# Optimization experiments

Measured on AMD Instinct MI355X. Metric: run time of the kernel, lower is better.

Reference implementation:

```python
import jax, jax.numpy as jnp
import numpy as np
from jax import lax

IMAGE_SIZE = 1280
STRIDE = 32
FMP = IMAGE_SIZE // STRIDE          # 40
BPC = 5                             # boxes per cell (5 anchors)
NUM_CLASSES = 80
NMS_THRESH = 0.5
CONF_THRESH = 0.3
N_BOX = FMP * FMP * BPC             # 8000 candidates
ANCHOR_SIZE = np.array([[17, 25], [55, 75], [92, 206], [202, 21], [289, 311]], dtype=np.float32)


def _make_anchors():
    # generate_anchors: per-cell (x,y) grid repeated for each of BPC anchors, tiled anchor wh
    ys, xs = jnp.meshgrid(jnp.arange(FMP, dtype=jnp.float32), jnp.arange(FMP, dtype=jnp.float32), indexing='ij')
    xy = jnp.stack([xs, ys], axis=-1).reshape(-1, 1, 2)                       # [HW,1,2]
    anchor_xy = jnp.broadcast_to(xy, (FMP * FMP, BPC, 2)).reshape(-1, 2)      # [N,2]
    anchor_wh = jnp.broadcast_to(jnp.asarray(ANCHOR_SIZE)[None], (FMP * FMP, BPC, 2)).reshape(-1, 2)
    return jnp.concatenate([anchor_xy, anchor_wh], axis=-1)                   # [N,4]


def setup_inputs() -> dict:
    key = jax.random.key(0)
    k = jax.random.split(key, 5)
    return {
        'cls_feat': jax.random.normal(k[0], (1, 512, FMP, FMP), jnp.float32),
        'reg_feat': jax.random.normal(k[1], (1, 512, FMP, FMP), jnp.float32),
        'w_obj': jax.random.normal(k[2], (BPC, 512), jnp.float32) * 0.02,
        'b_obj': jnp.zeros((BPC,), jnp.float32),
        'w_cls': jax.random.normal(k[3], (NUM_CLASSES * BPC, 512), jnp.float32) * 0.02,
        'b_cls': jnp.zeros((NUM_CLASSES * BPC,), jnp.float32),
        'w_reg': jax.random.normal(k[4], (4 * BPC, 512), jnp.float32) * 0.02,
        'b_reg': jnp.zeros((4 * BPC,), jnp.float32),
    }


def reference(cls_feat, reg_feat, w_obj, b_obj, w_cls, b_cls, w_reg, b_reg):
    # 1x1 convs as channel contractions, already permuted to NHWC like permute(0,2,3,1)
    obj = (jnp.einsum('bchw,oc->bhwo', reg_feat, w_obj) + b_obj).reshape(-1, 1)            # [N,1]
    cls = (jnp.einsum('bchw,oc->bhwo', cls_feat, w_cls) + b_cls).reshape(-1, NUM_CLASSES)  # [N,C]
    reg = (jnp.einsum('bchw,oc->bhwo', reg_feat, w_reg) + b_reg).reshape(-1, 4)            # [N,4]

    scores = jnp.sqrt(jax.nn.sigmoid(obj) * jax.nn.sigmoid(cls))                           # [N,C]

    # decode_boxes
    anchors = _make_anchors()
    ctr = (jax.nn.sigmoid(reg[:, :2]) + anchors[:, :2]) * STRIDE
    wh = jnp.exp(reg[:, 2:]) * anchors[:, 2:]
    bboxes = jnp.concatenate([ctr - wh * 0.5, ctr + wh * 0.5], axis=-1)                    # [N,4] x1y1x2y2

    # postprocess: per-box best class + confidence filter
    labels = jnp.argmax(scores, axis=1)
    score = jnp.take_along_axis(scores, labels[:, None], axis=1)[:, 0]
    valid = score >= CONF_THRESH

    # faithful to original nms(): it re-interprets decoded x1y1x2y2 as cxcywh before IoU
    b2 = jnp.concatenate([bboxes[:, :2] - bboxes[:, 2:] * 0.5,
                          bboxes[:, :2] + bboxes[:, 2:] * 0.5], axis=-1)

    # greedy per-class NMS == global greedy with cross-class IoU gated to 0
    order = jnp.argsort(-score)
    bs = b2[order]
    ls = labels[order]
    vs = valid[order]
    areas = (bs[:, 2] - bs[:, 0]) * (bs[:, 3] - bs[:, 1])
    xx1 = jnp.maximum(bs[:, None, 0], bs[None, :, 0])
    yy1 = jnp.maximum(bs[:, None, 1], bs[None, :, 1])
    xx2 = jnp.minimum(bs[:, None, 2], bs[None, :, 2])
    yy2 = jnp.minimum(bs[:, None, 3], bs[None, :, 3])
    inter = jnp.maximum(1e-10, xx2 - xx1) * jnp.maximum(1e-10, yy2 - yy1)
    iou = inter / (areas[:, None] + areas[None, :] - inter + 1e-14)                        # [N,N]
    same = ls[:, None] == ls[None, :]

    idx = jnp.arange(N_BOX)

    def body(k, supp):
        active = vs[k] & jnp.logical_not(supp[k])
        row = active & (iou[k] > NMS_THRESH) & same[k] & (idx > k)
        return supp | row

    supp = lax.fori_loop(0, N_BOX, body, jnp.zeros(N_BOX, bool))
    keep = jnp.zeros(N_BOX, bool).at[order].set(vs & jnp.logical_not(supp))

    # fixed-size masked outputs (original returns variable-length filtered arrays)
    return bboxes, score, labels, keep
```

## Files before the change

### kernel.cpp

```cpp
#include <hip/hip_runtime.h>
#include <math.h>

#define FMPX 40
#define NPOS 1600
#define NCLS 80
#define NBOX 8000
#define KDIM 512
#define CAP  256

__constant__ float c_aw[5] = {17.f, 55.f, 92.f, 202.f, 289.f};
__constant__ float c_ah[5] = {25.f, 75.f, 206.f, 21.f, 311.f};

__device__ __forceinline__ float sigf(float x) { return 1.0f / (1.0f + expf(-x)); }

__global__ __launch_bounds__(256) void k_gemm(
    const float* __restrict__ cls_feat, const float* __restrict__ reg_feat,
    const float* __restrict__ w_obj, const float* __restrict__ b_obj,
    const float* __restrict__ w_cls, const float* __restrict__ b_cls,
    const float* __restrict__ w_reg, const float* __restrict__ b_reg,
    float* __restrict__ clsRaw,
    float* __restrict__ roRaw)
{
    __shared__ float Ws[16 * KDIM];
    const int mTile = blockIdx.x;
    const int nTile = blockIdx.y;
    const int hw0   = mTile * 64;
    const bool isCls = (nTile < 25);
    const float* feat = isCls ? cls_feat : reg_feat;

    const int pos = threadIdx.x & 63;
    const int og  = threadIdx.x >> 6;

    const float* ap = feat + hw0 + pos;

    float A0[8], A1[8];
#pragma unroll
    for (int t = 0; t < 8; t++) A0[t] = ap[t * NPOS];
#pragma unroll
    for (int t = 0; t < 8; t++) A1[t] = ap[(8 + t) * NPOS];

    for (int i = threadIdx.x * 4; i < 16 * KDIM; i += 256 * 4) {
        int r = i >> 9, k = i & 511;
        const float* src;
        bool valid = true;
        if (isCls) {
            src = w_cls + (nTile * 16 + r) * KDIM + k;
        } else {
            int o = (nTile - 25) * 16 + r;
            if (o < 5)       src = w_obj + o * KDIM + k;
            else if (o < 25) src = w_reg + (o - 5) * KDIM + k;
            else           { src = w_obj; valid = false; }
        }
        float4 v = valid ? *(const float4*)src : make_float4(0.f, 0.f, 0.f, 0.f);
        *(float4*)&Ws[i] = v;
    }

    float bias[4];
    bool ok[4];
#pragma unroll
    for (int j = 0; j < 4; j++) {
        int r = og * 4 + j;
        if (isCls) {
            bias[j] = b_cls[nTile * 16 + r]; ok[j] = true;
        } else {
            int o = (nTile - 25) * 16 + r;
            if (o < 5)       { bias[j] = b_obj[o];     ok[j] = true; }
            else if (o < 25) { bias[j] = b_reg[o - 5]; ok[j] = true; }
            else             { bias[j] = 0.0f;         ok[j] = false; }
        }
    }

    __syncthreads();

    float acc[4] = {0.f, 0.f, 0.f, 0.f};
    const float* wsBase = &Ws[(og * 4) * KDIM];

    for (int kk = 0; kk < KDIM - 16; kk += 16) {
#pragma unroll
        for (int j = 0; j < 4; j++) {
            const float* wp = wsBase + j * KDIM + kk;
            acc[j] += A0[0] * wp[0]; acc[j] += A0[1] * wp[1];
            acc[j] += A0[2] * wp[2]; acc[j] += A0[3] * wp[3];
            acc[j] += A0[4] * wp[4]; acc[j] += A0[5] * wp[5];
            acc[j] += A0[6] * wp[6]; acc[j] += A0[7] * wp[7];
        }
#pragma unroll
        for (int t = 0; t < 8; t++) A0[t] = ap[(kk + 16 + t) * NPOS];
#pragma unroll
        for (int j = 0; j < 4; j++) {
            const float* wp = wsBase + j * KDIM + kk + 8;
            acc[j] += A1[0] * wp[0]; acc[j] += A1[1] * wp[1];
            acc[j] += A1[2] * wp[2]; acc[j] += A1[3] * wp[3];
            acc[j] += A1[4] * wp[4]; acc[j] += A1[5] * wp[5];
            acc[j] += A1[6] * wp[6]; acc[j] += A1[7] * wp[7];
        }
#pragma unroll
        for (int t = 0; t < 8; t++) A1[t] = ap[(kk + 24 + t) * NPOS];
    }
    {
        const int kk = KDIM - 16;
#pragma unroll
        for (int j = 0; j < 4; j++) {
            const float* wp = wsBase + j * KDIM + kk;
            acc[j] += A0[0] * wp[0]; acc[j] += A0[1] * wp[1];
            acc[j] += A0[2] * wp[2]; acc[j] += A0[3] * wp[3];
            acc[j] += A0[4] * wp[4]; acc[j] += A0[5] * wp[5];
            acc[j] += A0[6] * wp[6]; acc[j] += A0[7] * wp[7];
        }
#pragma unroll
        for (int j = 0; j < 4; j++) {
            const float* wp = wsBase + j * KDIM + kk + 8;
            acc[j] += A1[0] * wp[0]; acc[j] += A1[1] * wp[1];
            acc[j] += A1[2] * wp[2]; acc[j] += A1[3] * wp[3];
            acc[j] += A1[4] * wp[4]; acc[j] += A1[5] * wp[5];
            acc[j] += A1[6] * wp[6]; acc[j] += A1[7] * wp[7];
        }
    }

    const int hw = hw0 + pos;
    if (isCls) {
        float4 rv = make_float4(acc[0] + bias[0], acc[1] + bias[1],
                                acc[2] + bias[2], acc[3] + bias[3]);
        *(float4*)&clsRaw[hw * 400 + nTile * 16 + og * 4] = rv;
    } else {
#pragma unroll
        for (int j = 0; j < 4; j++) {
            int o = (nTile - 25) * 16 + og * 4 + j;
            if (ok[j]) roRaw[hw * 25 + o] = acc[j] + bias[j];
        }
    }
}

__global__ __launch_bounds__(256) void k_box(
    const float* __restrict__ clsRaw, const float* __restrict__ roRaw,
    float* __restrict__ out,
    float4* __restrict__ nmsBox, float* __restrict__ nmsArea,
    float2* __restrict__ sl)
{
    const int n = blockIdx.x * 4 + (threadIdx.x >> 6);
    const int lane = threadIdx.x & 63;
    const int hw = n / 5, a = n % 5;

    const float sobj = sigf(roRaw[hw * 25 + a]);
    const float* cbase = clsRaw + hw * 400 + a * 80;

    const int l4 = (lane < 20) ? lane : 19;
    float4 cs = *(const float4*)(cbase + l4 * 4);

    float s0 = sqrtf(sobj * sigf(cs.x));
    float s1 = sqrtf(sobj * sigf(cs.y));
    float s2 = sqrtf(sobj * sigf(cs.z));
    float s3 = sqrtf(sobj * sigf(cs.w));
    float v = s0; int bi = l4 * 4;
    if (s1 > v) { v = s1; bi = l4 * 4 + 1; }
    if (s2 > v) { v = s2; bi = l4 * 4 + 2; }
    if (s3 > v) { v = s3; bi = l4 * 4 + 3; }
    if (lane >= 20) { v = -1.0f; bi = 0x7FFFFFFF; }

#pragma unroll
    for (int off = 32; off >= 1; off >>= 1) {
        float ov = __shfl_xor(v, off);
        int   oi = __shfl_xor(bi, off);
        if (ov > v || (ov == v && oi < bi)) { v = ov; bi = oi; }
    }

    if (lane == 0) {
        const float* rp = roRaw + hw * 25 + 5 + a * 4;
        float r0 = rp[0], r1 = rp[1], r2 = rp[2], r3 = rp[3];
        float gx = (float)(hw % FMPX), gy = (float)(hw / FMPX);
        float cx = (sigf(r0) + gx) * 32.0f;
        float cy = (sigf(r1) + gy) * 32.0f;
        float wv = expf(r2) * c_aw[a];
        float hv = expf(r3) * c_ah[a];
        float x1 = cx - wv * 0.5f, y1 = cy - hv * 0.5f;
        float x2 = cx + wv * 0.5f, y2 = cy + hv * 0.5f;

        out[n * 4 + 0] = x1; out[n * 4 + 1] = y1;
        out[n * 4 + 2] = x2; out[n * 4 + 3] = y2;
        out[32000 + n] = v;
        out[40000 + n] = (float)bi;
        out[48000 + n] = 0.0f;
        sl[n] = make_float2(v, (float)bi);

        float nx1 = x1 - x2 * 0.5f, ny1 = y1 - y2 * 0.5f;
        float nx2 = x1 + x2 * 0.5f, ny2 = y1 + y2 * 0.5f;
        nmsBox[n]  = make_float4(nx1, ny1, nx2, ny2);
        nmsArea[n] = (nx2 - nx1) * (ny2 - ny1);
    }
}

__global__ __launch_bounds__(256) void k_nms(
    const float2* __restrict__ sl,
    const float4* __restrict__ nmsBox, const float* __restrict__ nmsArea,
    float* __restrict__ keepOut)
{
    const int c = blockIdx.x;

    __shared__ float ss[CAP];
    __shared__ int   si[CAP];
    __shared__ float bx1[CAP], by1[CAP], bx2[CAP], by2[CAP], bar[CAP];
    __shared__ int   supp[CAP];
    __shared__ int   cnt;

    if (threadIdx.x == 0) cnt = 0;
    __syncthreads();

    for (int i = threadIdx.x; i < NBOX; i += 256) {
        float2 p = sl[i];
        if (p.x >= 0.3f && (int)p.y == c) {
            int q = atomicAdd(&cnt, 1);
            if (q < CAP) { ss[q] = p.x; si[q] = i; }
        }
    }
    __syncthreads();

    int m = cnt;
    if (m > CAP) m = CAP;

    int P = 2;
    while (P < m) P <<= 1;
    for (int i = threadIdx.x; i < P; i += 256) {
        if (i >= m) { ss[i] = -INFINITY; si[i] = 0x7FFFFFFF; }
    }
    __syncthreads();

    for (int size = 2; size <= P; size <<= 1) {
        for (int stride = size >> 1; stride > 0; stride >>= 1) {
            for (int t = threadIdx.x; t < P / 2; t += 256) {
                int lo = 2 * stride * (t / stride) + (t % stride);
                int hi = lo + stride;
                bool desc = ((lo & size) == 0);
                float slo = ss[lo], shi = ss[hi];
                int   ilo = si[lo], ihi = si[hi];
                bool loBetter = (slo > shi) || (slo == shi && ilo < ihi);
                bool doSwap = desc ? !loBetter : loBetter;
                if (doSwap) { ss[lo] = shi; ss[hi] = slo; si[lo] = ihi; si[hi] = ilo; }
            }
            __syncthreads();
        }
    }

    for (int i = threadIdx.x; i < m; i += 256) {
        int n = si[i];
        float4 b = nmsBox[n];
        bx1[i] = b.x; by1[i] = b.y; bx2[i] = b.z; by2[i] = b.w;
        bar[i] = nmsArea[n];
        supp[i] = 0;
    }
    __syncthreads();

    for (int k = 0; k < m; k++) {
        if (!supp[k]) {
            float kx1 = bx1[k], ky1 = by1[k], kx2 = bx2[k], ky2 = by2[k], ka = bar[k];
            for (int j = k + 1 + threadIdx.x; j < m; j += 256) {
                float xx1 = fmaxf(kx1, bx1[j]);
                float yy1 = fmaxf(ky1, by1[j]);
                float xx2 = fminf(kx2, bx2[j]);
                float yy2 = fminf(ky2, by2[j]);
                float inter = fmaxf(1e-10f, xx2 - xx1) * fmaxf(1e-10f, yy2 - yy1);
                float iou = inter / ((ka + bar[j] - inter) + 1e-14f);
                if (iou > 0.5f) supp[j] = 1;
            }
        }
        __syncthreads();
    }

    for (int j = threadIdx.x; j < m; j += 256) {
        if (!supp[j]) keepOut[si[j]] = 1.0f;
    }
}

extern "C" void kernel_launch(void* const* d_in, const int* in_sizes, int n_in,
                              void* d_out, int out_size, void* d_ws, size_t ws_size,
                              hipStream_t stream) {
    const float* cls_feat = (const float*)d_in[0];
    const float* reg_feat = (const float*)d_in[1];
    const float* w_obj    = (const float*)d_in[2];
    const float* b_obj    = (const float*)d_in[3];
    const float* w_cls    = (const float*)d_in[4];
    const float* b_cls    = (const float*)d_in[5];
    const float* w_reg    = (const float*)d_in[6];
    const float* b_reg    = (const float*)d_in[7];

    float* out = (float*)d_out;
    float* ws  = (float*)d_ws;

    float*  clsRaw    = ws;
    float*  roRaw     = ws + 640000;
    float4* nmsBox    = (float4*)(ws + 680000);
    float*  nmsArea   = ws + 712000;
    float2* sl        = (float2*)(ws + 720000);

    k_gemm<<<dim3(25, 27), 256, 0, stream>>>(cls_feat, reg_feat,
                                             w_obj, b_obj, w_cls, b_cls, w_reg, b_reg,
                                             clsRaw, roRaw);
    k_box<<<NBOX / 4, 256, 0, stream>>>(clsRaw, roRaw, out, nmsBox, nmsArea, sl);
    k_nms<<<NCLS, 256, 0, stream>>>(sl, nmsBox, nmsArea, out + 48000);
}
```

Before: 150.0 us.

## Replace sort-then-NMS with single-wavefront argmax-select NMS in registers

The per-class NMS kernel no longer runs a shared-memory bitonic sort followed by a sequential suppression loop with a block barrier per candidate. A single 64-lane wavefront instead holds up to 256 candidates in registers. Each round it finds the highest remaining score with a shuffle reduction, keeps that box, broadcasts its coordinates, and suppresses overlapping boxes locally. This removes every __syncthreads and most shared-memory traffic, but leaves 192 threads idle and does a wave-wide reduction for every kept box.

After: 188.0 us. 25.3% more time.

```diff
diff --git a/kernel.cpp b/kernel.cpp
--- a/kernel.cpp
+++ b/kernel.cpp
@@ -198,8 +198,6 @@
 
     __shared__ float ss[CAP];
     __shared__ int   si[CAP];
-    __shared__ float bx1[CAP], by1[CAP], bx2[CAP], by2[CAP], bar[CAP];
-    __shared__ int   supp[CAP];
     __shared__ int   cnt;
 
     if (threadIdx.x == 0) cnt = 0;
@@ -214,59 +212,75 @@
     }
     __syncthreads();
 
+    if (threadIdx.x >= 64) return;
+    const int lane = threadIdx.x;
     int m = cnt;
     if (m > CAP) m = CAP;
 
-    int P = 2;
-    while (P < m) P <<= 1;
-    for (int i = threadIdx.x; i < P; i += 256) {
-        if (i >= m) { ss[i] = -INFINITY; si[i] = 0x7FFFFFFF; }
-    }
-    __syncthreads();
-
-    for (int size = 2; size <= P; size <<= 1) {
-        for (int stride = size >> 1; stride > 0; stride >>= 1) {
-            for (int t = threadIdx.x; t < P / 2; t += 256) {
-                int lo = 2 * stride * (t / stride) + (t % stride);
-                int hi = lo + stride;
-                bool desc = ((lo & size) == 0);
-                float slo = ss[lo], shi = ss[hi];
-                int   ilo = si[lo], ihi = si[hi];
-                bool loBetter = (slo > shi) || (slo == shi && ilo < ihi);
-                bool doSwap = desc ? !loBetter : loBetter;
-                if (doSwap) { ss[lo] = shi; ss[hi] = slo; si[lo] = ihi; si[hi] = ilo; }
+    float s[4]; int id[4];
+    float x1[4], y1[4], x2[4], y2[4], ar[4];
+#pragma unroll
+    for (int r = 0; r < 4; r++) {
+        int t = r * 64 + lane;
+        if (t < m) {
+            s[r] = ss[t]; id[r] = si[t];
+            float4 b = nmsBox[id[r]];
+            x1[r] = b.x; y1[r] = b.y; x2[r] = b.z; y2[r] = b.w;
+            ar[r] = nmsArea[id[r]];
+        } else {
+            s[r] = -INFINITY; id[r] = 0x7FFFFFFF;
+            x1[r] = 0.f; y1[r] = 0.f; x2[r] = 0.f; y2[r] = 0.f; ar[r] = 0.f;
+        }
+    }
+
+    for (int it = 0; it < m; it++) {
+        float bs = s[0]; int bi = id[0]; int bc = 0;
+#pragma unroll
+        for (int r = 1; r < 4; r++) {
+            if (s[r] > bs || (s[r] == bs && id[r] < bi)) { bs = s[r]; bi = id[r]; bc = r; }
+        }
+        bc |= (lane << 2);
+#pragma unroll
+        for (int off = 32; off >= 1; off >>= 1) {
+            float os = __shfl_xor(bs, off);
+            int   oi = __shfl_xor(bi, off);
+            int   oc = __shfl_xor(bc, off);
+            if (os > bs || (os == bs && oi < bi)) { bs = os; bi = oi; bc = oc; }
+        }
+        if (bs == -INFINITY) break;
+
+        const int wl = bc >> 2, wr = bc & 3;
+        float tx1 = (wr == 0) ? x1[0] : (wr == 1) ? x1[1] : (wr == 2) ? x1[2] : x1[3];
+        float ty1 = (wr == 0) ? y1[0] : (wr == 1) ? y1[1] : (wr == 2) ? y1[2] : y1[3];
+        float tx2 = (wr == 0) ? x2[0] : (wr == 1) ? x2[1] : (wr == 2) ? x2[2] : x2[3];
+        float ty2 = (wr == 0) ? y2[0] : (wr == 1) ? y2[1] : (wr == 2) ? y2[2] : y2[3];
+        float tar = (wr == 0) ? ar[0] : (wr == 1) ? ar[1] : (wr == 2) ? ar[2] : ar[3];
+        const float kx1 = __shfl(tx1, wl);
+        const float ky1 = __shfl(ty1, wl);
+        const float kx2 = __shfl(tx2, wl);
+        const float ky2 = __shfl(ty2, wl);
+        const float ka  = __shfl(tar, wl);
+
+        if (lane == wl) {
+            keepOut[bi] = 1.0f;
+            if      (wr == 0) s[0] = -INFINITY;
+            else if (wr == 1) s[1] = -INFINITY;
+            else if (wr == 2) s[2] = -INFINITY;
+            else              s[3] = -INFINITY;
+        }
+
+#pragma unroll
+        for (int r = 0; r < 4; r++) {
+            if (s[r] != -INFINITY) {
+                float xx1 = fmaxf(kx1, x1[r]);
+                float yy1 = fmaxf(ky1, y1[r]);
+                float xx2 = fminf(kx2, x2[r]);
+                float yy2 = fminf(ky2, y2[r]);
+                float inter = fmaxf(1e-10f, xx2 - xx1) * fmaxf(1e-10f, yy2 - yy1);
+                float iou = inter / ((ka + ar[r] - inter) + 1e-14f);
+                if (iou > 0.5f) s[r] = -INFINITY;
             }
-            __syncthreads();
-        }
-    }
-
-    for (int i = threadIdx.x; i < m; i += 256) {
-        int n = si[i];
-        float4 b = nmsBox[n];
-        bx1[i] = b.x; by1[i] = b.y; bx2[i] = b.z; by2[i] = b.w;
-        bar[i] = nmsArea[n];
-        supp[i] = 0;
-    }
-    __syncthreads();
-
-    for (int k = 0; k < m; k++) {
-        if (!supp[k]) {
-            float kx1 = bx1[k], ky1 = by1[k], kx2 = bx2[k], ky2 = by2[k], ka = bar[k];
-            for (int j = k + 1 + threadIdx.x; j < m; j += 256) {
-                float xx1 = fmaxf(kx1, bx1[j]);
-                float yy1 = fmaxf(ky1, by1[j]);
-                float xx2 = fminf(kx2, bx2[j]);
-                float yy2 = fminf(ky2, by2[j]);
-                float inter = fmaxf(1e-10f, xx2 - xx1) * fmaxf(1e-10f, yy2 - yy1);
-                float iou = inter / ((ka + bar[j] - inter) + 1e-14f);
-                if (iou > 0.5f) supp[j] = 1;
-            }
-        }
-        __syncthreads();
-    }
-
-    for (int j = threadIdx.x; j < m; j += 256) {
-        if (!supp[j]) keepOut[si[j]] = 1.0f;
+        }
     }
 }
 
```
